# Performance work log

Measured on AMD Instinct MI355X. Metric: run time of the kernel, lower is better.

Reference implementation:

```python
import jax, jax.numpy as jnp
import numpy as np
import math

D_MODEL = 2048
D_STATE = 16
EXPAND = 2
D_INNER = D_MODEL * EXPAND          # 4096
DT_RANK = math.ceil(D_MODEL / 16)   # 128
BATCH, SEQ_LEN = 2, 512


def setup_inputs() -> dict:
    key = jax.random.key(0)
    ks = jax.random.split(key, 6)
    x = jax.random.normal(ks[0], (BATCH, SEQ_LEN, D_INNER), dtype=jnp.float32)
    # A_log such that A = -exp(A_log) is a stable negative-real decay
    A_log = jnp.log(jax.random.uniform(ks[1], (D_INNER, D_STATE), minval=0.5, maxval=16.0, dtype=jnp.float32))
    D = jnp.ones((D_INNER,), dtype=jnp.float32)
    x_proj_w = 0.02 * jax.random.normal(ks[2], (DT_RANK + 2 * D_STATE, D_INNER), dtype=jnp.float32)
    dt_init_std = DT_RANK ** -0.5
    dt_proj_w = jax.random.uniform(ks[3], (D_INNER, DT_RANK), minval=-dt_init_std, maxval=dt_init_std, dtype=jnp.float32)
    # inverse-softplus init of dt bias, dt ~ loguniform[1e-3, 0.1]
    dt = jnp.exp(jax.random.uniform(ks[4], (D_INNER,), dtype=jnp.float32) * (math.log(0.1) - math.log(0.001)) + math.log(0.001))
    dt = jnp.clip(dt, 1e-4, None)
    dt_proj_b = dt + jnp.log(-jnp.expm1(-dt))
    return {"x": x, "A_log": A_log, "D": D, "x_proj_w": x_proj_w,
            "dt_proj_w": dt_proj_w, "dt_proj_b": dt_proj_b}


def reference(x, A_log, D, x_proj_w, dt_proj_w, dt_proj_b):
    # x: (b, l, d)
    A = -jnp.exp(A_log)                                  # (d, n)
    xp = jnp.einsum('bld,rd->blr', x, x_proj_w)          # (b, l, dt_rank + 2n)
    dt_in = xp[..., :DT_RANK]
    B = xp[..., DT_RANK:DT_RANK + D_STATE]               # (b, l, n)
    C = xp[..., DT_RANK + D_STATE:]                      # (b, l, n)
    dt = jax.nn.softplus(jnp.einsum('blr,dr->bld', dt_in, dt_proj_w) + dt_proj_b)  # (b, l, d)
    dA = jnp.exp(dt[..., None] * A)                      # (b, l, d, n)
    dBx = dt[..., None] * B[:, :, None, :] * x[..., None]  # (b, l, d, n)

    def step(h, inp):
        dA_t, dBx_t, C_t = inp                           # (b,d,n), (b,d,n), (b,n)
        h = dA_t * h + dBx_t
        y = jnp.einsum('bdn,bn->bd', h, C_t)
        return h, y

    h0 = jnp.zeros((x.shape[0], D_INNER, D_STATE), dtype=x.dtype)
    _, ys = jax.lax.scan(step, h0,
                         (jnp.moveaxis(dA, 1, 0), jnp.moveaxis(dBx, 1, 0), jnp.moveaxis(C, 1, 0)))
    y = jnp.moveaxis(ys, 0, 1) + D * x                   # (b, l, d)
    return y
```

## Files before the change

kernel.cpp:

```cpp
#include <hip/hip_runtime.h>
#include <math.h>

#define BATCH   2
#define SEQLEN  512
#define DI      4096
#define DS      16
#define RDT     128
#define RTOT    160
#define BL      1024

#define KSP     8

#define LOG2E 1.44269504088896340736f
#define LN2   0.69314718055994530942f

typedef __bf16 bf16;
typedef bf16  bf16x8 __attribute__((ext_vector_type(8)));
typedef bf16  bf16x4 __attribute__((ext_vector_type(4)));
typedef float f32x4  __attribute__((ext_vector_type(4)));

__device__ __forceinline__ bf16x8 cvt8(const float4 a, const float4 b) {
  bf16x8 r;
  r[0] = (bf16)a.x; r[1] = (bf16)a.y; r[2] = (bf16)a.z; r[3] = (bf16)a.w;
  r[4] = (bf16)b.x; r[5] = (bf16)b.y; r[6] = (bf16)b.z; r[7] = (bf16)b.w;
  return r;
}

__device__ __forceinline__ bf16x8 cvt8s(const float4 a, const float4 b, const float s) {
  bf16x8 r;
  r[0] = (bf16)(s * a.x); r[1] = (bf16)(s * a.y); r[2] = (bf16)(s * a.z); r[3] = (bf16)(s * a.w);
  r[4] = (bf16)(s * b.x); r[5] = (bf16)(s * b.y); r[6] = (bf16)(s * b.z); r[7] = (bf16)(s * b.w);
  return r;
}

#define LPAD 164

__global__ __launch_bounds__(512) void gemm_part(const float* __restrict__ x,
                                                 const float* __restrict__ W,
                                                 bf16* __restrict__ dtp,
                                                 float* __restrict__ bcp) {
  __shared__ float Lred[4][16 * LPAD];
  const int tid = threadIdx.x;
  const int w = tid >> 6;
  const int lane = tid & 63;
  const int m = lane & 15;
  const int q = lane >> 4;
  const int row0 = blockIdx.x * 16;
  const int ks = blockIdx.y;
  const int k0 = ks * (DI / KSP) + w * 64;

  f32x4 acc[10] = {};
  const float* ap = x + (size_t)(row0 + m) * DI + k0 + 8 * q;
  const float* wp = W + (size_t)m * DI + k0 + 8 * q;

#pragma unroll
  for (int kk = 0; kk < 64; kk += 32) {
    float4 a0 = *(const float4*)(ap + kk);
    float4 a1 = *(const float4*)(ap + kk + 4);
    bf16x8 af = cvt8(a0, a1);
#pragma unroll
    for (int nt = 0; nt < 10; ++nt) {
      const float* wq = wp + (size_t)nt * 16 * DI + kk;
      float4 b0 = *(const float4*)(wq);
      float4 b1 = *(const float4*)(wq + 4);
      acc[nt] = __builtin_amdgcn_mfma_f32_16x16x32_bf16(af, cvt8(b0, b1), acc[nt], 0, 0, 0);
    }
  }

  if (w < 4) {
#pragma unroll
    for (int nt = 0; nt < 10; ++nt)
#pragma unroll
      for (int r = 0; r < 4; ++r)
        Lred[w][(4 * q + r) * LPAD + nt * 16 + m] = acc[nt][r];
  }
  __syncthreads();
  if (w >= 4) {
#pragma unroll
    for (int nt = 0; nt < 10; ++nt)
#pragma unroll
      for (int r = 0; r < 4; ++r)
        Lred[w - 4][(4 * q + r) * LPAD + nt * 16 + m] += acc[nt][r];
  }
  __syncthreads();

#pragma unroll
  for (int i = 0; i < 5; ++i) {
    const int o = i * 512 + tid;
    const int row = o / 160;
    const int col = o - row * 160;
    const int a = row * LPAD + col;
    const float s = Lred[0][a] + Lred[1][a] + Lred[2][a] + Lred[3][a];
    if (col < RDT) dtp[(size_t)ks * (BL * RDT) + (size_t)(row0 + row) * RDT + col] = (bf16)s;
    else           bcp[(size_t)ks * (BL * 32) + (size_t)(row0 + row) * 32 + (col - RDT)] = s;
  }
}

__global__ __launch_bounds__(256) void reduce_slabs(const bf16* __restrict__ dtp,
                                                    const float* __restrict__ bcp,
                                                    bf16* __restrict__ dtin,
                                                    float* __restrict__ BCf) {
  const int o = (blockIdx.x * 256 + threadIdx.x) * 4;
  const int row = o / RTOT;
  const int col = o - row * RTOT;
  if (col < RDT) {
    float s0 = 0.f, s1 = 0.f, s2 = 0.f, s3 = 0.f;
#pragma unroll
    for (int ks = 0; ks < KSP; ++ks) {
      bf16x4 v = *(const bf16x4*)(dtp + (size_t)ks * (BL * RDT) + (size_t)row * RDT + col);
      s0 += (float)v[0]; s1 += (float)v[1]; s2 += (float)v[2]; s3 += (float)v[3];
    }
    bf16x4 ob;
    ob[0] = (bf16)s0; ob[1] = (bf16)s1; ob[2] = (bf16)s2; ob[3] = (bf16)s3;
    *(bf16x4*)(dtin + (size_t)row * RDT + col) = ob;
  } else {
    float4 s = make_float4(0.f, 0.f, 0.f, 0.f);
#pragma unroll
    for (int ks = 0; ks < KSP; ++ks) {
      float4 v = *(const float4*)&bcp[(size_t)ks * (BL * 32) + (size_t)row * 32 + (col - RDT)];
      s.x += v.x; s.y += v.y; s.z += v.z; s.w += v.w;
    }
    *(float4*)&BCf[(size_t)row * 32 + (col - RDT)] = s;
  }
}

__device__ __forceinline__ float row16_reduce_add(float p) {
  p += __int_as_float(__builtin_amdgcn_update_dpp(
      0, __float_as_int(p), 0x111, 0xf, 0xf, true));
  p += __int_as_float(__builtin_amdgcn_update_dpp(
      0, __float_as_int(p), 0x112, 0xf, 0xf, true));
  p += __int_as_float(__builtin_amdgcn_update_dpp(
      0, __float_as_int(p), 0x114, 0xf, 0xf, true));
  p += __int_as_float(__builtin_amdgcn_update_dpp(
      0, __float_as_int(p), 0x118, 0xf, 0xf, true));
  return p;
}

#define TC  64
#define TCP 68
#define NCH (SEQLEN / TC)

__global__ __launch_bounds__(256) void scan_fused(const float* __restrict__ x,
                                                  const float* __restrict__ A_log,
                                                  const float* __restrict__ Dvec,
                                                  const float* __restrict__ BCf,
                                                  const bf16* __restrict__ dtin,
                                                  const float* __restrict__ dtw,
                                                  const float* __restrict__ dtb,
                                                  float* __restrict__ out) {
  __shared__ __align__(16) float dtS[16][TCP];
  __shared__ __align__(16) float uS[16][TCP];
  __shared__ __align__(16) float BS[16][TCP];
  __shared__ __align__(16) float CS[16][TCP];
  __shared__ __align__(16) float yS[TC][16];

  const int bid = blockIdx.x;
  const int b = bid >> 8;
  const int d0 = (bid & 255) * 16;
  const int tid = threadIdx.x;
  const int n = tid & 15;
  const int dc = tid >> 4;
  const int d = d0 + dc;
  const int w = tid >> 6;
  const int m = tid & 15;
  const int q = (tid >> 4) & 3;

  const float A2 = -LOG2E * __expf(A_log[d * DS + n]);
  const float bias2 = dtb[d0 + m] * LOG2E;

  bf16x8 bfragW[4];
#pragma unroll
  for (int k = 0; k < 4; ++k) {
    const float* p = dtw + (size_t)(d0 + m) * RDT + 32 * k + 8 * q;
    float4 w0 = *(const float4*)p;
    float4 w1 = *(const float4*)(p + 4);
    bfragW[k] = cvt8s(w0, w1, LOG2E);
  }

  const int lt = tid >> 2;
  const int lf = (tid & 3) * 4;
  const int rowbase = b * SEQLEN;
  const float4 Dv4 = *(const float4*)&Dvec[d0 + lf];

  const int xtrow = rowbase + 16 * w + 4 * q;

  bf16x8 afrag[4];
  float xm[4];
  float4 rx, rB, rC, rx_prev;
  {
    const int arow = rowbase + 16 * w + m;
#pragma unroll
    for (int k = 0; k < 4; ++k)
      afrag[k] = *(const bf16x8*)(dtin + (size_t)arow * RDT + 32 * k + 8 * q);
#pragma unroll
    for (int r = 0; r < 4; ++r)
      xm[r] = x[(size_t)(xtrow + r) * DI + d0 + m];
    const int row = rowbase + lt;
    rx = *(const float4*)&x[(size_t)row * DI + d0 + lf];
    rB = *(const float4*)&BCf[row * 32 + lf];
    rC = *(const float4*)&BCf[row * 32 + 16 + lf];
  }

  float h = 0.f;

  for (int c = 0; c < NCH; ++c) {
    if (c > 0) __syncthreads();

    {
      f32x4 acc = {};
#pragma unroll
      for (int k = 0; k < 4; ++k)
        acc = __builtin_amdgcn_mfma_f32_16x16x32_bf16(afrag[k], bfragW[k], acc, 0, 0, 0);
#pragma unroll
      for (int r = 0; r < 4; ++r) {
        const float z2 = acc[r] + bias2;
        const float dts =
            (z2 > 28.854f) ? z2 * LN2
                           : LN2 * __builtin_amdgcn_logf(1.f + __builtin_amdgcn_exp2f(z2));
        dtS[m][16 * w + 4 * q + r] = dts;
        uS[m][16 * w + 4 * q + r] = dts * xm[r];
      }
    }
    {
      const float rBa[4] = {rB.x, rB.y, rB.z, rB.w};
      const float rCa[4] = {rC.x, rC.y, rC.z, rC.w};
#pragma unroll
      for (int j = 0; j < 4; ++j) {
        BS[lf + j][lt] = rBa[j];
        CS[lf + j][lt] = rCa[j];
      }
    }
    if (c > 0) {
      const int prow = rowbase + (c - 1) * TC + lt;
      float4 yv = *(const float4*)&yS[lt][lf];
      float4 o4;
      o4.x = fmaf(Dv4.x, rx_prev.x, yv.x);
      o4.y = fmaf(Dv4.y, rx_prev.y, yv.y);
      o4.z = fmaf(Dv4.z, rx_prev.z, yv.z);
      o4.w = fmaf(Dv4.w, rx_prev.w, yv.w);
      *(float4*)&out[(size_t)prow * DI + d0 + lf] = o4;
    }
    rx_prev = rx;

    __syncthreads();

    if (c < NCH - 1) {
      const int arow = rowbase + (c + 1) * TC + 16 * w + m;
#pragma unroll
      for (int k = 0; k < 4; ++k)
        afrag[k] = *(const bf16x8*)(dtin + (size_t)arow * RDT + 32 * k + 8 * q);
#pragma unroll
      for (int r = 0; r < 4; ++r)
        xm[r] = x[(size_t)(xtrow + (c + 1) * TC + r) * DI + d0 + m];
      const int row = rowbase + (c + 1) * TC + lt;
      rx = *(const float4*)&x[(size_t)row * DI + d0 + lf];
      rB = *(const float4*)&BCf[row * 32 + lf];
      rC = *(const float4*)&BCf[row * 32 + 16 + lf];
    }

    __builtin_amdgcn_s_setprio(1);
#pragma unroll
    for (int g = 0; g < 8; ++g) {
      const int t0 = 8 * g;
      const float4 dv0 = *(const float4*)&dtS[dc][t0];
      const float4 dv1 = *(const float4*)&dtS[dc][t0 + 4];
      const float4 uv0 = *(const float4*)&uS[dc][t0];
      const float4 uv1 = *(const float4*)&uS[dc][t0 + 4];
      const float4 Bv0 = *(const float4*)&BS[n][t0];
      const float4 Bv1 = *(const float4*)&BS[n][t0 + 4];
      const float4 Cv0 = *(const float4*)&CS[n][t0];
      const float4 Cv1 = *(const float4*)&CS[n][t0 + 4];
      const float dt[8] = {dv0.x, dv0.y, dv0.z, dv0.w, dv1.x, dv1.y, dv1.z, dv1.w};
      const float uv[8] = {uv0.x, uv0.y, uv0.z, uv0.w, uv1.x, uv1.y, uv1.z, uv1.w};
      const float Bv[8] = {Bv0.x, Bv0.y, Bv0.z, Bv0.w, Bv1.x, Bv1.y, Bv1.z, Bv1.w};
      const float Cv[8] = {Cv0.x, Cv0.y, Cv0.z, Cv0.w, Cv1.x, Cv1.y, Cv1.z, Cv1.w};

      float e[8], u[8], p[8];
#pragma unroll
      for (int j = 0; j < 8; ++j) {
        e[j] = __builtin_amdgcn_exp2f(dt[j] * A2);
        u[j] = uv[j] * Bv[j];
      }
#pragma unroll
      for (int j = 0; j < 8; ++j) {
        h = fmaf(e[j], h, u[j]);
        p[j] = h * Cv[j];
      }
#pragma unroll
      for (int j = 0; j < 8; ++j)
        p[j] = row16_reduce_add(p[j]);
      if (n == 15) {
#pragma unroll
        for (int j = 0; j < 8; ++j)
          yS[t0 + j][dc] = p[j];
      }
    }
    __builtin_amdgcn_s_setprio(0);
  }

  __syncthreads();
  {
    const int prow = rowbase + (NCH - 1) * TC + lt;
    float4 yv = *(const float4*)&yS[lt][lf];
    float4 o4;
    o4.x = fmaf(Dv4.x, rx_prev.x, yv.x);
    o4.y = fmaf(Dv4.y, rx_prev.y, yv.y);
    o4.z = fmaf(Dv4.z, rx_prev.z, yv.z);
    o4.w = fmaf(Dv4.w, rx_prev.w, yv.w);
    *(float4*)&out[(size_t)prow * DI + d0 + lf] = o4;
  }
}

extern "C" void kernel_launch(void* const* d_in, const int* in_sizes, int n_in,
                              void* d_out, int out_size, void* d_ws, size_t ws_size,
                              hipStream_t stream) {
  const float* x     = (const float*)d_in[0];
  const float* A_log = (const float*)d_in[1];
  const float* Dv    = (const float*)d_in[2];
  const float* W     = (const float*)d_in[3];
  const float* dtw   = (const float*)d_in[4];
  const float* dtb   = (const float*)d_in[5];
  float* out = (float*)d_out;

  char* ws = (char*)d_ws;
  bf16*  dtp  = (bf16*)ws;
  float* bcp  = (float*)(ws + (size_t)KSP * BL * RDT * sizeof(bf16));
  bf16*  dtin = (bf16*)(ws + (size_t)KSP * BL * RDT * sizeof(bf16)
                           + (size_t)KSP * BL * 32 * sizeof(float));
  float* BCf  = (float*)(ws + (size_t)KSP * BL * RDT * sizeof(bf16)
                            + (size_t)KSP * BL * 32 * sizeof(float)
                            + (size_t)BL * RDT * sizeof(bf16));

  gemm_part<<<dim3(64, KSP), 512, 0, stream>>>(x, W, dtp, bcp);
  reduce_slabs<<<dim3(160), 256, 0, stream>>>(dtp, bcp, dtin, BCf);
  scan_fused<<<dim3(512), 256, 0, stream>>>(x, A_log, Dv, BCf, dtin, dtw, dtb, out);
}
```

Measured before the change: 135.5 us.

## Split gemm_part work by output column tiles instead of K to drop LDS reduction

The x-projection GEMM partial kernel now gives each of 5 waves two 16-column output tiles over the block's full 512-wide K slice, instead of 8 waves each covering a 64-wide K chunk for all 10 tiles. This removes the shared-memory cross-wave reduction, the two barriers and the LDS footprint, and lets each wave store its results directly. In exchange, every wave reloads and converts the same x rows (five times redundant A loads), each wave runs a longer serial K loop with only two accumulators, and there are fewer waves per block.

```diff
diff --git a/kernel.cpp b/kernel.cpp
--- a/kernel.cpp
+++ b/kernel.cpp
@@ -33,13 +33,10 @@
   return r;
 }
 
-#define LPAD 164
-
-__global__ __launch_bounds__(512) void gemm_part(const float* __restrict__ x,
+__global__ __launch_bounds__(320) void gemm_part(const float* __restrict__ x,
                                                  const float* __restrict__ W,
                                                  bf16* __restrict__ dtp,
                                                  float* __restrict__ bcp) {
-  __shared__ float Lred[4][16 * LPAD];
   const int tid = threadIdx.x;
   const int w = tid >> 6;
   const int lane = tid & 63;
@@ -47,52 +44,42 @@
   const int q = lane >> 4;
   const int row0 = blockIdx.x * 16;
   const int ks = blockIdx.y;
-  const int k0 = ks * (DI / KSP) + w * 64;
-
-  f32x4 acc[10] = {};
-  const float* ap = x + (size_t)(row0 + m) * DI + k0 + 8 * q;
-  const float* wp = W + (size_t)m * DI + k0 + 8 * q;
-
-#pragma unroll
-  for (int kk = 0; kk < 64; kk += 32) {
-    float4 a0 = *(const float4*)(ap + kk);
-    float4 a1 = *(const float4*)(ap + kk + 4);
-    bf16x8 af = cvt8(a0, a1);
-#pragma unroll
-    for (int nt = 0; nt < 10; ++nt) {
-      const float* wq = wp + (size_t)nt * 16 * DI + kk;
-      float4 b0 = *(const float4*)(wq);
-      float4 b1 = *(const float4*)(wq + 4);
-      acc[nt] = __builtin_amdgcn_mfma_f32_16x16x32_bf16(af, cvt8(b0, b1), acc[nt], 0, 0, 0);
-    }
-  }
-
-  if (w < 4) {
-#pragma unroll
-    for (int nt = 0; nt < 10; ++nt)
-#pragma unroll
-      for (int r = 0; r < 4; ++r)
-        Lred[w][(4 * q + r) * LPAD + nt * 16 + m] = acc[nt][r];
-  }
-  __syncthreads();
-  if (w >= 4) {
-#pragma unroll
-    for (int nt = 0; nt < 10; ++nt)
-#pragma unroll
-      for (int r = 0; r < 4; ++r)
-        Lred[w - 4][(4 * q + r) * LPAD + nt * 16 + m] += acc[nt][r];
-  }
-  __syncthreads();
-
-#pragma unroll
-  for (int i = 0; i < 5; ++i) {
-    const int o = i * 512 + tid;
-    const int row = o / 160;
-    const int col = o - row * 160;
-    const int a = row * LPAD + col;
-    const float s = Lred[0][a] + Lred[1][a] + Lred[2][a] + Lred[3][a];
-    if (col < RDT) dtp[(size_t)ks * (BL * RDT) + (size_t)(row0 + row) * RDT + col] = (bf16)s;
-    else           bcp[(size_t)ks * (BL * 32) + (size_t)(row0 + row) * 32 + (col - RDT)] = s;
+  const int k0 = ks * (DI / KSP);
+  const int ntA = 2 * w;
+  const int ntB = 2 * w + 1;
+
+  f32x4 accA = {}, accB = {};
+  const float* ap  = x + (size_t)(row0 + m) * DI + k0 + 8 * q;
+  const float* wpA = W + (size_t)(ntA * 16 + m) * DI + k0 + 8 * q;
+  const float* wpB = W + (size_t)(ntB * 16 + m) * DI + k0 + 8 * q;
+
+#pragma unroll 4
+  for (int kk = 0; kk < 512; kk += 32) {
+    bf16x8 af = cvt8(*(const float4*)(ap + kk),  *(const float4*)(ap + kk + 4));
+    bf16x8 bA = cvt8(*(const float4*)(wpA + kk), *(const float4*)(wpA + kk + 4));
+    bf16x8 bB = cvt8(*(const float4*)(wpB + kk), *(const float4*)(wpB + kk + 4));
+    accA = __builtin_amdgcn_mfma_f32_16x16x32_bf16(af, bA, accA, 0, 0, 0);
+    accB = __builtin_amdgcn_mfma_f32_16x16x32_bf16(af, bB, accB, 0, 0, 0);
+  }
+
+  if (ntA < 8) {
+    bf16* dA = dtp + (size_t)ks * (BL * RDT) + ntA * 16 + m;
+    bf16* dB = dtp + (size_t)ks * (BL * RDT) + ntB * 16 + m;
+#pragma unroll
+    for (int r = 0; r < 4; ++r) {
+      const size_t row = row0 + 4 * q + r;
+      dA[row * RDT] = (bf16)accA[r];
+      dB[row * RDT] = (bf16)accB[r];
+    }
+  } else {
+    float* bA = bcp + (size_t)ks * (BL * 32) + m;
+    float* bB = bcp + (size_t)ks * (BL * 32) + 16 + m;
+#pragma unroll
+    for (int r = 0; r < 4; ++r) {
+      const size_t row = row0 + 4 * q + r;
+      bA[row * 32] = accA[r];
+      bB[row * 32] = accB[r];
+    }
   }
 }
 
@@ -331,7 +318,7 @@
                             + (size_t)KSP * BL * 32 * sizeof(float)
                             + (size_t)BL * RDT * sizeof(bf16));
 
-  gemm_part<<<dim3(64, KSP), 512, 0, stream>>>(x, W, dtp, bcp);
+  gemm_part<<<dim3(64, KSP), 320, 0, stream>>>(x, W, dtp, bcp);
   reduce_slabs<<<dim3(160), 256, 0, stream>>>(dtp, bcp, dtin, BCf);
   scan_fused<<<dim3(512), 256, 0, stream>>>(x, A_log, Dv, BCf, dtin, dtw, dtb, out);
 }
```

Measured after the change: 140.0 us. 3.3% more time.
